# Optimization experiments

Hardware: AMD Instinct MI355X
Metric: run time of the kernel (lower is better)

Reference implementation:

```python
import jax, jax.numpy as jnp
import numpy as np

B, H, W = 4, 112, 112
N = H * W              # 12544 tokens
NBHD = 48              # local neighborhood size
DIM = 256
OUT_DIM = 512
INNER = 4              # inner_ch of weight_net
TABLE = 4096           # pre_table rows
ALPHA = 4.0
DS_RATE = 0.25
STRIDE = 2
RESERVE = (H // 4) * (W // 4)  # 784 reserve tokens (pos % 4 == 0)
EPS = 1e-5


def _ln(x, g, b):
    m = x.mean(-1, keepdims=True)
    v = ((x - m) ** 2).mean(-1, keepdims=True)
    return (x - m) / jnp.sqrt(v + EPS) * g + b


def setup_inputs() -> dict:
    key = jax.random.key(0)
    ks = jax.random.split(key, 8)
    ii, jj = jnp.meshgrid(jnp.arange(H), jnp.arange(W), indexing='ij')
    pos = jnp.stack([ii, jj], -1).reshape(1, N, 2).astype(jnp.float32)
    pos = jnp.tile(pos, (B, 1, 1))                             # b x n x 2 integer grid
    feat = jax.random.normal(ks[0], (B, N, DIM), jnp.float32)
    member_idx = jax.random.randint(ks[1], (B, N, NBHD), 0, N)
    cluster_mask = (jax.random.uniform(ks[2], (B, N, NBHD)) > 0.1).astype(jnp.float32)
    learned_prob = jax.random.uniform(ks[3], (B, N, 1), dtype=jnp.float32)
    pe_idx = jax.random.randint(ks[4], (B, N, NBHD), 0, TABLE)
    pre_table = jax.random.normal(ks[5], (TABLE, 5), jnp.float32)
    w1 = jax.random.normal(ks[6], (5, INNER), jnp.float32) * 0.4
    b1 = jnp.zeros((INNER,), jnp.float32)
    ln1_g = jnp.ones((INNER,), jnp.float32)
    ln1_b = jnp.zeros((INNER,), jnp.float32)
    norm_g = jnp.ones((INNER * DIM,), jnp.float32)
    norm_b = jnp.zeros((INNER * DIM,), jnp.float32)
    lin_w = jax.random.normal(ks[7], (INNER * DIM, OUT_DIM), jnp.float32) * (1.0 / np.sqrt(INNER * DIM))
    lin_b = jnp.zeros((OUT_DIM,), jnp.float32)
    return dict(pos=pos, feat=feat, member_idx=member_idx, cluster_mask=cluster_mask,
                learned_prob=learned_prob, stride=STRIDE, pe_idx=pe_idx, reserve_num=RESERVE,
                pre_table=pre_table, w1=w1, b1=b1, ln1_g=ln1_g, ln1_b=ln1_b,
                norm_g=norm_g, norm_b=norm_b, lin_w=lin_w, lin_b=lin_b)


def reference(pos, feat, member_idx, cluster_mask, learned_prob, stride, pe_idx,
              reserve_num, pre_table, w1, b1, ln1_g, ln1_b, norm_g, norm_b, lin_w, lin_b):
    b, n, c = feat.shape
    keep_num = int(n * DS_RATE)
    pos_long = pos.astype(jnp.int32)
    # stride == 2 branch: tokens on the coarse grid get prob 1
    grid_prob = jnp.all(pos_long % stride == 0, axis=-1).astype(jnp.float32)      # b x n
    lp_s = jax.lax.stop_gradient(learned_prob).reshape(b, n) * ALPHA              # detached scores
    final_prob = grid_prob + lp_s
    reserve_mask = jnp.all(pos_long % (stride * 2) == 0, axis=-1).astype(jnp.float32)
    final_prob = final_prob + reserve_mask * (-100.0)
    sample_num = keep_num - reserve_num
    _, sample_idx = jax.lax.top_k(final_prob, sample_num)                         # b x sample_num
    # per-row nonzero of reserve_mask (exactly reserve_num hits per row)
    flat_nz = jnp.nonzero(reserve_mask.reshape(-1) > 0, size=b * reserve_num)[0]
    reserve_idx = (flat_nz % n).reshape(b, reserve_num).astype(sample_idx.dtype)
    idx = jnp.concatenate([sample_idx, reserve_idx], axis=1)                      # b x keep_num

    pos_k = jnp.take_along_axis(pos, idx[:, :, None], axis=1)                     # b x keep x 2
    nbhd = member_idx.shape[-1]
    mem_k = jnp.take_along_axis(member_idx, idx[:, :, None], axis=1)              # b x keep x nbhd
    pe_k = jnp.take_along_axis(pe_idx, idx[:, :, None], axis=1)
    cm_k = jnp.take_along_axis(cluster_mask, idx[:, :, None], axis=1)
    lp = jnp.take_along_axis(learned_prob, mem_k.reshape(b, -1, 1), axis=1)
    lp = lp.reshape(b, keep_num, nbhd, 1)

    # weight_net on the small PE table, then gather per-edge weights
    wt = jax.nn.gelu(_ln(pre_table @ w1 + b1, ln1_g, ln1_b), approximate=False)   # TABLE x INNER
    weights = wt[pe_k]                                                            # b x keep x nbhd x INNER
    weights = weights * (lp * cm_k[..., None])

    # CLUSTENWF: gather neighbor features and weighted-sum over the neighborhood
    gathered = jnp.take_along_axis(feat, mem_k.reshape(b, -1, 1), axis=1)
    gathered = gathered.reshape(b, keep_num, nbhd, c)                             # b x keep x nbhd x c
    out = jnp.einsum('bnkm,bnkc->bnmc', weights, gathered).reshape(b, keep_num, INNER * c)
    out = _ln(out, norm_g, norm_b)
    return pos_k, out @ lin_w + lin_b
```

## Files before the change

### kernel.cpp

```cpp
#include <hip/hip_runtime.h>

typedef unsigned short u16;
typedef unsigned int u32;
typedef unsigned long long u64;

#define NB 4
#define NTOK 12544
#define NBHD 48
#define DIM 256
#define OUTD 512
#define KEEPN 3136
#define SAMPLEN 2352
#define RESN 784
#define GW 112
#define TABLE 4096
#define POSN (NB * KEEPN * 2)
#define QTR (NTOK / 4)
#define NBKT 16384

#define BLKM 128
#define BLKN 256
#define BROW 40

#define FEATB_BYTES (25690112ull)
#define XWS_BYTES   (25690112ull)
#define LINT_BYTES  (1048576ull)
#define KEYS_BYTES  (401408ull)
#define PART_BYTES  (802816ull)
#define WS_NEED (FEATB_BYTES + XWS_BYTES + LINT_BYTES + KEYS_BYTES + PART_BYTES)

__device__ __forceinline__ float bf2f(u16 u) {
    union { u32 i; float f; } v; v.i = ((u32)u) << 16; return v.f;
}
__device__ __forceinline__ float asf(u32 u) {
    union { u32 i; float f; } v; v.i = u; return v.f;
}
__device__ __forceinline__ u16 f2bf(float f) {
    union { u32 i; float f; } v; v.f = f;
    return (u16)((v.i + 0x7FFFu + ((v.i >> 16) & 1u)) >> 16);
}

typedef __bf16 bf16x8 __attribute__((ext_vector_type(8)));
typedef float floatx4 __attribute__((ext_vector_type(4)));
typedef float floatx2 __attribute__((ext_vector_type(2)));

__device__ __forceinline__ float make_f(float lp, int n) {
    int i = n / GW, j = n % GW;
    float f = lp * 4.0f;
    if (((i | j) & 1) == 0) f = 1.0f + f;
    if (((i | j) & 3) == 0) f = f + (-100.0f);
    return f;
}
__device__ __forceinline__ u64 f_to_key(float f, int n) {
    union { float f; u32 u; } v; v.f = f;
    u32 m = (v.u & 0x80000000u) ? ~v.u : (v.u | 0x80000000u);
    return (((u64)m) << 32) | (u64)(0xFFFFFFFFu - (u32)n);
}
__device__ __forceinline__ int f_to_bucket(float f) {
    int b = (int)floorf(f * 3276.8f);
    return b < 0 ? 0 : (b > NBKT - 1 ? NBKT - 1 : b);
}

__global__ __launch_bounds__(256) void prep_kernel(
    const float* __restrict__ feat, u16* __restrict__ featb,
    const float* __restrict__ lin_w, u16* __restrict__ linT,
    u32* __restrict__ hist,
    const float* __restrict__ pre_table, const float* __restrict__ w1,
    const float* __restrict__ b1, const float* __restrict__ g1,
    const float* __restrict__ bb1, float* __restrict__ wt) {
    __shared__ u16 T[64 * 65];
    int bid = blockIdx.x;
    int t = threadIdx.x;
    if (bid >= 128) {
        int ft = (bid - 128) * 256 + t;
        float4 v = ((const float4*)feat)[ft];
        u64 w = (u64)f2bf(v.x) | ((u64)f2bf(v.y) << 16) |
                ((u64)f2bf(v.z) << 32) | ((u64)f2bf(v.w) << 48);
        ((u64*)featb)[ft] = w;
        return;
    }
    int bx = bid & 15, by = bid >> 4;
    int k0 = bx * 64, n0 = by * 64;
    hist[bid * 512 + t] = 0;
    hist[bid * 512 + 256 + t] = 0;
    int gid = bid * 256 + t;
    if (gid < TABLE) {
        float z[4];
#pragma unroll
        for (int m = 0; m < 4; ++m) {
            float acc = b1[m];
#pragma unroll
            for (int d = 0; d < 5; ++d) acc += pre_table[gid * 5 + d] * w1[d * 4 + m];
            z[m] = acc;
        }
        float mean = (z[0] + z[1] + z[2] + z[3]) * 0.25f;
        float var = 0.0f;
#pragma unroll
        for (int m = 0; m < 4; ++m) { float d = z[m] - mean; var += d * d; }
        float rstd = rsqrtf(var * 0.25f + 1e-5f);
        float wv[4];
#pragma unroll
        for (int m = 0; m < 4; ++m) {
            float y = (z[m] - mean) * rstd * g1[m] + bb1[m];
            wv[m] = 0.5f * y * (1.0f + erff(y * 0.70710678118654752f));
        }
        *(float4*)&wt[gid * 4] = make_float4(wv[0], wv[1], wv[2], wv[3]);
    }
    int r = t >> 2, c4 = (t & 3) * 16;
#pragma unroll
    for (int i = 0; i < 4; ++i) {
        float4 v = *(const float4*)&lin_w[(size_t)(k0 + r) * OUTD + n0 + c4 + i * 4];
        T[(c4 + i * 4 + 0) * 65 + r] = f2bf(v.x);
        T[(c4 + i * 4 + 1) * 65 + r] = f2bf(v.y);
        T[(c4 + i * 4 + 2) * 65 + r] = f2bf(v.z);
        T[(c4 + i * 4 + 3) * 65 + r] = f2bf(v.w);
    }
    __syncthreads();
    int nl = t >> 2, kc = (t & 3) * 16;
    union { uint4 v[2]; u16 h[16]; } u;
#pragma unroll
    for (int i = 0; i < 16; ++i) u.h[i] = T[nl * 65 + kc + i];
    u16* dst = &linT[(size_t)(n0 + nl) * 1024 + k0 + kc];
    *(uint4*)(dst + 0) = u.v[0];
    *(uint4*)(dst + 8) = u.v[1];
}

__global__ __launch_bounds__(256) void hist_kernel(
    const float* __restrict__ lprob, u32* __restrict__ hist) {
    int g = blockIdx.x * 256 + threadIdx.x;
    int b = g / NTOK, n = g % NTOK;
    int bkt = f_to_bucket(make_f(lprob[g], n));
    atomicAdd(&hist[b * NBKT + bkt], 1u);
}

__global__ __launch_bounds__(1024) void prefix_kernel(
    const u32* __restrict__ hist, u32* __restrict__ base, u32* __restrict__ cursor) {
    int b = blockIdx.x, t = threadIdx.x;
    const u32* h = hist + b * NBKT;
    u32 loc[16], own = 0;
#pragma unroll
    for (int i = 0; i < 16; ++i) { loc[i] = h[t * 16 + i]; own += loc[i]; }
    __shared__ u32 buf[2][1024];
    buf[0][t] = own;
    __syncthreads();
    int src = 0;
    for (int off = 1; off < 1024; off <<= 1) {
        u32 v = buf[src][t] + ((t + off < 1024) ? buf[src][t + off] : 0u);
        buf[src ^ 1][t] = v;
        src ^= 1;
        __syncthreads();
    }
    u32 above = buf[src][t] - own;
    u32 suf = 0, bout[16];
    for (int i = 15; i >= 0; --i) { bout[i] = above + suf; suf += loc[i]; }
    u32* bb = base + b * NBKT;
    u32* cc = cursor + b * NBKT;
#pragma unroll
    for (int i = 0; i < 16; ++i) { bb[t * 16 + i] = bout[i]; cc[t * 16 + i] = bout[i]; }
}

__global__ __launch_bounds__(256) void scatter_kernel(
    const float* __restrict__ lprob, u32* __restrict__ cursor,
    u64* __restrict__ slots) {
    int g = blockIdx.x * 256 + threadIdx.x;
    int b = g / NTOK, n = g % NTOK;
    float f = make_f(lprob[g], n);
    int bkt = f_to_bucket(f);
    u32 s = atomicAdd(&cursor[b * NBKT + bkt], 1u);
    slots[b * NTOK + s] = f_to_key(f, n);
}

__global__ __launch_bounds__(256) void rank_finalize_kernel(
    const float* __restrict__ lprob, const u32* __restrict__ hist,
    const u32* __restrict__ base, const u64* __restrict__ slots,
    float* __restrict__ pos_out) {
    int g = blockIdx.x * 256 + threadIdx.x;
    int b = g / NTOK, n = g % NTOK;
    int i = n / GW, j = n % GW;
    if (((i | j) & 3) == 0) {
        int r = (i >> 2) * 28 + (j >> 2);
        int slot = b * KEEPN + SAMPLEN + r;
        pos_out[slot * 2 + 0] = (float)i;
        pos_out[slot * 2 + 1] = (float)j;
        return;
    }
    float f = make_f(lprob[g], n);
    int bkt = f_to_bucket(f);
    u32 r0 = base[b * NBKT + bkt];
    if (r0 >= SAMPLEN) return;
    u64 my = f_to_key(f, n);
    u32 cnt = hist[b * NBKT + bkt];
    const u64* sl = slots + b * NTOK + r0;
    u32 rank = r0;
    for (u32 s = 0; s < cnt; ++s) rank += (sl[s] > my) ? 1u : 0u;
    if (rank < SAMPLEN) {
        int slot = b * KEEPN + (int)rank;
        pos_out[slot * 2 + 0] = (float)i;
        pos_out[slot * 2 + 1] = (float)j;
    }
}

__global__ __launch_bounds__(1024, 2) void token_v10_kernel(
    const float* __restrict__ pos_in, u16* __restrict__ xdst,
    const int* __restrict__ member_idx, const int* __restrict__ pe_idx,
    const float* __restrict__ cmask, const float* __restrict__ lprob,
    const u16* __restrict__ featb, const float* __restrict__ wt,
    const float* __restrict__ norm_g, const float* __restrict__ norm_b) {
    int bi = blockIdx.x;
    int xcd = bi & 7, jj = bi >> 3;
    int b = xcd >> 1;
    int tid = threadIdx.x;
    int wave = tid >> 6, lane = tid & 63;
    int t = b * KEEPN + (xcd & 1) * 1568 + jj * 16 + wave;

    __shared__ float4 w_s[16][NBHD];

    float2 pp = *(const float2*)&pos_in[t * 2];
    int n_src = (int)pp.x * GW + (int)pp.y;

    u32 moffb = 0;
    if (lane < NBHD) {
        int e = (b * NTOK + n_src) * NBHD + lane;
        int mem = member_idx[e];
        float sc = lprob[b * NTOK + mem] * cmask[e];
        float4 w4 = *(const float4*)&wt[pe_idx[e] * 4];
        w_s[wave][lane] = make_float4(w4.x * sc, w4.y * sc, w4.z * sc, w4.w * sc);
        moffb = (u32)mem * (DIM * 2);
    }
    __syncthreads();

    floatx2 accA[4] = {};
    floatx2 accB[4] = {};
    const char* fb = (const char*)featb + (size_t)b * NTOK * DIM * 2;
    u32 lane8 = (u32)lane * 8;
#pragma unroll
    for (int k = 0; k < NBHD; ++k) {
        u32 mk = (u32)__builtin_amdgcn_readlane((int)moffb, k);
        uint2 d = *(const uint2*)(fb + mk + lane8);
        float4 w = w_s[wave][k];
        floatx2 w01 = {w.x, w.y};
        floatx2 w23 = {w.z, w.w};
        float c0 = asf(d.x << 16);
        float c1 = asf(d.x & 0xFFFF0000u);
        float c2 = asf(d.y << 16);
        float c3 = asf(d.y & 0xFFFF0000u);
        floatx2 c0v = {c0, c0}, c1v = {c1, c1}, c2v = {c2, c2}, c3v = {c3, c3};
        accA[0] = __builtin_elementwise_fma(w01, c0v, accA[0]);
        accB[0] = __builtin_elementwise_fma(w23, c0v, accB[0]);
        accA[1] = __builtin_elementwise_fma(w01, c1v, accA[1]);
        accB[1] = __builtin_elementwise_fma(w23, c1v, accB[1]);
        accA[2] = __builtin_elementwise_fma(w01, c2v, accA[2]);
        accB[2] = __builtin_elementwise_fma(w23, c2v, accB[2]);
        accA[3] = __builtin_elementwise_fma(w01, c3v, accA[3]);
        accB[3] = __builtin_elementwise_fma(w23, c3v, accB[3]);
    }

    float s1 = 0.0f, s2 = 0.0f;
#pragma unroll
    for (int j = 0; j < 4; ++j) {
        float v0 = accA[j][0], v1 = accA[j][1], v2 = accB[j][0], v3 = accB[j][1];
        s1 += v0 + v1 + v2 + v3;
        s2 += v0 * v0 + v1 * v1 + v2 * v2 + v3 * v3;
    }
#pragma unroll
    for (int off = 32; off > 0; off >>= 1) {
        s1 += __shfl_xor(s1, off, 64);
        s2 += __shfl_xor(s2, off, 64);
    }
    float mean = s1 * (1.0f / 1024.0f);
    float var = fmaxf(s2 * (1.0f / 1024.0f) - mean * mean, 0.0f);
    float rstd = rsqrtf(var + 1e-5f);

    u16* Xp = xdst + (size_t)t * 1024;
#pragma unroll
    for (int m = 0; m < 4; ++m) {
        int cc = m * 256 + lane * 4;
        float4 g4 = *(const float4*)&norm_g[cc];
        float4 b4 = *(const float4*)&norm_b[cc];
        float v0 = (m == 0) ? accA[0][0] : (m == 1) ? accA[0][1]
                 : (m == 2) ? accB[0][0] : accB[0][1];
        float v1 = (m == 0) ? accA[1][0] : (m == 1) ? accA[1][1]
                 : (m == 2) ? accB[1][0] : accB[1][1];
        float v2 = (m == 0) ? accA[2][0] : (m == 1) ? accA[2][1]
                 : (m == 2) ? accB[2][0] : accB[2][1];
        float v3 = (m == 0) ? accA[3][0] : (m == 1) ? accA[3][1]
                 : (m == 2) ? accB[3][0] : accB[3][1];
        u16 h0 = f2bf((v0 - mean) * rstd * g4.x + b4.x);
        u16 h1 = f2bf((v1 - mean) * rstd * g4.y + b4.y);
        u16 h2 = f2bf((v2 - mean) * rstd * g4.z + b4.z);
        u16 h3 = f2bf((v3 - mean) * rstd * g4.w + b4.w);
        u64 w = (u64)h0 | ((u64)h1 << 16) | ((u64)h2 << 32) | ((u64)h3 << 48);
        *(u64*)(Xp + cc) = w;
    }
}

#define GROW 40
__global__ __launch_bounds__(256) void gemm_tile_kernel(
    const u16* __restrict__ xws, const u16* __restrict__ linT,
    const float* __restrict__ lin_b, float* __restrict__ out) {
    __shared__ __align__(16) u16 As[128 * GROW];
    __shared__ __align__(16) u16 Bs[64 * GROW];
    int bid = blockIdx.x;
    int xcd = bid & 7, c = bid >> 3;
    int tile = xcd * 98 + c;
    int m0 = (tile >> 3) * 128, n0 = (tile & 7) * 64;

    int tid = threadIdx.x;
    int wave = tid >> 6, lane = tid & 63;
    int l15 = lane & 15, quad = lane >> 4;
    int wm = wave >> 1, wn = wave & 1;
    int sr = tid >> 2, sk = (tid & 3) * 8;

    const u16* Ap0 = xws + (size_t)(m0 + sr) * 1024 + sk;
    const u16* Ap1 = Ap0 + (size_t)64 * 1024;
    const u16* Bp0 = linT + (size_t)(n0 + sr) * 1024 + sk;

    uint4 a0 = *(const uint4*)(Ap0);
    uint4 a1 = *(const uint4*)(Ap1);
    uint4 b0 = *(const uint4*)(Bp0);

    floatx4 acc[4][2] = {};
    for (int kk = 0; kk < 1024; kk += 32) {
        __syncthreads();
        *(uint4*)&As[sr * GROW + sk] = a0;
        *(uint4*)&As[(64 + sr) * GROW + sk] = a1;
        *(uint4*)&Bs[sr * GROW + sk] = b0;
        __syncthreads();
        if (kk + 32 < 1024) {
            a0 = *(const uint4*)(Ap0 + kk + 32);
            a1 = *(const uint4*)(Ap1 + kk + 32);
            b0 = *(const uint4*)(Bp0 + kk + 32);
        }
        bf16x8 af[4], bfv[2];
#pragma unroll
        for (int mi = 0; mi < 4; ++mi)
            af[mi] = *(const bf16x8*)&As[(wm * 64 + mi * 16 + l15) * GROW + quad * 8];
#pragma unroll
        for (int ni = 0; ni < 2; ++ni)
            bfv[ni] = *(const bf16x8*)&Bs[(wn * 32 + ni * 16 + l15) * GROW + quad * 8];
#pragma unroll
        for (int mi = 0; mi < 4; ++mi)
#pragma unroll
            for (int ni = 0; ni < 2; ++ni)
                acc[mi][ni] = __builtin_amdgcn_mfma_f32_16x16x32_bf16(
                    af[mi], bfv[ni], acc[mi][ni], 0, 0, 0);
    }
#pragma unroll
    for (int ni = 0; ni < 2; ++ni) {
        int col = n0 + wn * 32 + ni * 16 + l15;
        float bias = lin_b[col];
#pragma unroll
        for (int mi = 0; mi < 4; ++mi)
#pragma unroll
            for (int reg = 0; reg < 4; ++reg) {
                int row = m0 + wm * 64 + mi * 16 + quad * 4 + reg;
                out[(size_t)row * OUTD + col] = acc[mi][ni][reg] + bias;
            }
    }
}

__global__ __launch_bounds__(256) void key_kernel(
    const float* __restrict__ lprob, u64* __restrict__ keys) {
    int g = blockIdx.x * 256 + threadIdx.x;
    int n = g % NTOK;
    keys[g] = f_to_key(make_f(lprob[g], n), n);
}

__global__ __launch_bounds__(256) void partial_rank_kernel(
    const u64* __restrict__ keys, u32* __restrict__ part) {
    int b = blockIdx.y, z = blockIdx.z;
    int n = blockIdx.x * 256 + threadIdx.x;
    u64 my = keys[b * NTOK + n];
    const u64* kb = keys + b * NTOK + z * QTR;
    u32 cnt = 0;
    for (int t = 0; t < QTR; t += 8) {
#pragma unroll
        for (int j = 0; j < 8; ++j) cnt += (kb[t + j] > my) ? 1u : 0u;
    }
    part[(z * NB + b) * NTOK + n] = cnt;
}

__global__ __launch_bounds__(256) void finalize_kernel(
    const u32* __restrict__ part, float* __restrict__ pos_out) {
    int b = blockIdx.y;
    int n = blockIdx.x * 256 + threadIdx.x;
    int g = b * NTOK + n;
    u32 rank = part[g] + part[(NB + b) * NTOK + n] +
               part[(2 * NB + b) * NTOK + n] + part[(3 * NB + b) * NTOK + n];
    int i = n / GW, j = n % GW;
    if (rank < SAMPLEN) {
        int slot = b * KEEPN + (int)rank;
        pos_out[slot * 2 + 0] = (float)i;
        pos_out[slot * 2 + 1] = (float)j;
    }
    if (((i | j) & 3) == 0) {
        int r = (i >> 2) * 28 + (j >> 2);
        int slot = b * KEEPN + SAMPLEN + r;
        pos_out[slot * 2 + 0] = (float)i;
        pos_out[slot * 2 + 1] = (float)j;
    }
}

__global__ __launch_bounds__(256) void token_fb_kernel(
    const float* __restrict__ pos_in, u16* __restrict__ xdst,
    const int* __restrict__ member_idx, const int* __restrict__ pe_idx,
    const float* __restrict__ cmask, const float* __restrict__ lprob,
    const float* __restrict__ featf, const float* __restrict__ pre_table,
    const float* __restrict__ w1, const float* __restrict__ b1,
    const float* __restrict__ g1, const float* __restrict__ bb1,
    const float* __restrict__ norm_g, const float* __restrict__ norm_b) {
    int t = blockIdx.x;
    int b = t / KEEPN;
    int tid = threadIdx.x;
    __shared__ int mem_s[NBHD];
    __shared__ float4 w_s[NBHD];
    __shared__ float red[10];

    int n_src = (int)pos_in[t * 2 + 0] * GW + (int)pos_in[t * 2 + 1];

    if (tid < NBHD) {
        int e = (b * NTOK + n_src) * NBHD + tid;
        int mem = member_idx[e];
        int pe = pe_idx[e];
        float cm = cmask[e];
        float lpe = lprob[b * NTOK + mem];
        float z[4];
#pragma unroll
        for (int m = 0; m < 4; ++m) {
            float acc = b1[m];
#pragma unroll
            for (int d = 0; d < 5; ++d) acc += pre_table[pe * 5 + d] * w1[d * 4 + m];
            z[m] = acc;
        }
        float mean = (z[0] + z[1] + z[2] + z[3]) * 0.25f;
        float var = 0.0f;
#pragma unroll
        for (int m = 0; m < 4; ++m) { float d = z[m] - mean; var += d * d; }
        float rstd = rsqrtf(var * 0.25f + 1e-5f);
        float sc = lpe * cm;
        float wv[4];
#pragma unroll
        for (int m = 0; m < 4; ++m) {
            float y = (z[m] - mean) * rstd * g1[m] + bb1[m];
            wv[m] = 0.5f * y * (1.0f + erff(y * 0.70710678118654752f)) * sc;
        }
        w_s[tid] = make_float4(wv[0], wv[1], wv[2], wv[3]);
        mem_s[tid] = mem;
    }
    __syncthreads();

    float a0 = 0.f, a1 = 0.f, a2 = 0.f, a3 = 0.f;
    size_t base = (size_t)b * NTOK * DIM + tid;
#pragma unroll 8
    for (int k = 0; k < NBHD; ++k) {
        float g = featf[base + (size_t)mem_s[k] * DIM];
        float4 w = w_s[k];
        a0 += w.x * g; a1 += w.y * g; a2 += w.z * g; a3 += w.w * g;
    }
    float s1 = a0 + a1 + a2 + a3;
    float s2 = a0 * a0 + a1 * a1 + a2 * a2 + a3 * a3;
#pragma unroll
    for (int off = 32; off > 0; off >>= 1) {
        s1 += __shfl_down(s1, off, 64);
        s2 += __shfl_down(s2, off, 64);
    }
    int wave = tid >> 6, lane = tid & 63;
    if (lane == 0) { red[wave] = s1; red[4 + wave] = s2; }
    __syncthreads();
    if (tid == 0) {
        float S = red[0] + red[1] + red[2] + red[3];
        float Q = red[4] + red[5] + red[6] + red[7];
        float mean = S * (1.0f / 1024.0f);
        float var = fmaxf(Q * (1.0f / 1024.0f) - mean * mean, 0.0f);
        red[8] = mean; red[9] = rsqrtf(var + 1e-5f);
    }
    __syncthreads();
    float mean = red[8], rstd = red[9];
    float acc4[4] = {a0, a1, a2, a3};
    u16* Xp = xdst + (size_t)t * 1024;
#pragma unroll
    for (int m = 0; m < 4; ++m) {
        int cc = m * 256 + tid;
        float v = (acc4[m] - mean) * rstd * norm_g[cc] + norm_b[cc];
        Xp[cc] = f2bf(v);
    }
}

__global__ __launch_bounds__(256) void gemm_inplace_kernel(
    const float* __restrict__ lin_w, const float* __restrict__ lin_b,
    float* __restrict__ out) {
    __shared__ __align__(16) u16 Bs[BLKN * BROW];
    int tile_m = blockIdx.x;
    int nblk = blockIdx.y;
    int tid = threadIdx.x;
    int wave = tid >> 6, lane = tid & 63;
    int l15 = lane & 15, quad = lane >> 4;

    const u16* Xbase = (const u16*)out;
    floatx4 acc[8][4] = {};

    for (int kk = 0; kk < 1024; kk += 32) {
        __syncthreads();
#pragma unroll
        for (int it = 0; it < 4; ++it) {
            int task = it * 256 + tid;
            int kp = task >> 6;
            int ng = task & 63;
            int k = kp * 2;
            int n0 = nblk * BLKN + ng * 4;
            float4 fa = *(const float4*)&lin_w[(size_t)(kk + k) * OUTD + n0];
            float4 fb = *(const float4*)&lin_w[(size_t)(kk + k + 1) * OUTD + n0];
            u16* bp = &Bs[(ng * 4) * BROW + k];
            *(u32*)(bp + 0 * BROW) = (u32)f2bf(fa.x) | ((u32)f2bf(fb.x) << 16);
            *(u32*)(bp + 1 * BROW) = (u32)f2bf(fa.y) | ((u32)f2bf(fb.y) << 16);
            *(u32*)(bp + 2 * BROW) = (u32)f2bf(fa.z) | ((u32)f2bf(fb.z) << 16);
            *(u32*)(bp + 3 * BROW) = (u32)f2bf(fa.w) | ((u32)f2bf(fb.w) << 16);
        }
        __syncthreads();
        bf16x8 bfrag[4];
#pragma unroll
        for (int ni = 0; ni < 4; ++ni)
            bfrag[ni] = *(const bf16x8*)&Bs[(wave * 64 + ni * 16 + l15) * BROW + quad * 8];
#pragma unroll
        for (int mi = 0; mi < 8; ++mi) {
            int row = tile_m * BLKM + mi * 16 + l15;
            bf16x8 af = *(const bf16x8*)&Xbase[(size_t)row * 1024 + kk + quad * 8];
#pragma unroll
            for (int ni = 0; ni < 4; ++ni)
                acc[mi][ni] = __builtin_amdgcn_mfma_f32_16x16x32_bf16(
                    af, bfrag[ni], acc[mi][ni], 0, 0, 0);
        }
    }
    __syncthreads();
#pragma unroll
    for (int mi = 0; mi < 8; ++mi)
#pragma unroll
        for (int ni = 0; ni < 4; ++ni) {
            int col = nblk * BLKN + wave * 64 + ni * 16 + l15;
            float bias = lin_b[col];
#pragma unroll
            for (int reg = 0; reg < 4; ++reg) {
                int row = tile_m * BLKM + mi * 16 + quad * 4 + reg;
                out[(size_t)row * OUTD + col] = acc[mi][ni][reg] + bias;
            }
        }
}

extern "C" void kernel_launch(void* const* d_in, const int* in_sizes, int n_in,
                              void* d_out, int out_size, void* d_ws, size_t ws_size,
                              hipStream_t stream) {
    const float* feat     = (const float*)d_in[1];
    const int* member_idx = (const int*)d_in[2];
    const float* cmask    = (const float*)d_in[3];
    const float* lprob    = (const float*)d_in[4];
    const int* pe_idx     = (const int*)d_in[6];
    const float* pre_table= (const float*)d_in[8];
    const float* w1       = (const float*)d_in[9];
    const float* b1       = (const float*)d_in[10];
    const float* g1       = (const float*)d_in[11];
    const float* bb1      = (const float*)d_in[12];
    const float* norm_g   = (const float*)d_in[13];
    const float* norm_b   = (const float*)d_in[14];
    const float* lin_w    = (const float*)d_in[15];
    const float* lin_b    = (const float*)d_in[16];

    float* pos_out = (float*)d_out;
    float* out     = pos_out + POSN;

    if (ws_size >= WS_NEED) {
        char* ws = (char*)d_ws;
        u16* featb = (u16*)ws;
        u16* xws   = (u16*)(ws + FEATB_BYTES);
        u16* linT  = (u16*)(ws + FEATB_BYTES + XWS_BYTES);
        u64* slots = (u64*)(ws + FEATB_BYTES + XWS_BYTES + LINT_BYTES);
        u32* hist  = (u32*)(ws + FEATB_BYTES + XWS_BYTES + LINT_BYTES + KEYS_BYTES);
        u32* base  = hist + NB * NBKT;
        u32* curs  = base + NB * NBKT;
        float* wtbuf = out;

        prep_kernel<<<12672, 256, 0, stream>>>(
            feat, featb, lin_w, linT, hist, pre_table, w1, b1, g1, bb1, wtbuf);
        hist_kernel<<<(NB * NTOK) / 256, 256, 0, stream>>>(lprob, hist);
        prefix_kernel<<<NB, 1024, 0, stream>>>(hist, base, curs);
        scatter_kernel<<<(NB * NTOK) / 256, 256, 0, stream>>>(lprob, curs, slots);
        rank_finalize_kernel<<<(NB * NTOK) / 256, 256, 0, stream>>>(
            lprob, hist, base, slots, pos_out);
        token_v10_kernel<<<784, 1024, 0, stream>>>(
            pos_out, xws, member_idx, pe_idx, cmask, lprob, featb,
            wtbuf, norm_g, norm_b);
        gemm_tile_kernel<<<784, 256, 0, stream>>>(xws, linT, lin_b, out);
    } else {
        u64* keys = (u64*)out;
        u32* part = (u32*)((char*)out + 401408);

        key_kernel<<<(NB * NTOK) / 256, 256, 0, stream>>>(lprob, keys);
        partial_rank_kernel<<<dim3(49, NB, 4), 256, 0, stream>>>(keys, part);
        finalize_kernel<<<dim3(49, NB), 256, 0, stream>>>(part, pos_out);
        token_fb_kernel<<<NB * KEEPN, 256, 0, stream>>>(
            pos_out, (u16*)out, member_idx, pe_idx, cmask, lprob, feat,
            pre_table, w1, b1, g1, bb1, norm_g, norm_b);
        gemm_inplace_kernel<<<dim3(98, 2), 256, 0, stream>>>(lin_w, lin_b, out);
    }
}
```

Baseline: 245.3 us.

## Stage neighbor feature rows into LDS via async global_load_lds in two phases

The token aggregation kernel now copies the 48 gathered bf16 neighbor rows into LDS with direct global-to-LDS loads, issued as two batches of 24 rows. The second batch is issued after the first batch's compute, replacing per-iteration dependent global loads in the FMA loop. Blocks shrink from 1024 to 256 threads (4 tokens per block) to fit a roughly 48KB staging buffer per block. The aim is more memory-level parallelism for the irregular gather. The risk is lower occupancy from the LDS footprint, and overlap is limited because the second batch is waited on immediately.

New measurement: 248.3 us. No clear change (+1.2%).

```diff
diff --git a/kernel.cpp b/kernel.cpp
--- a/kernel.cpp
+++ b/kernel.cpp
@@ -43,6 +43,13 @@
 typedef __bf16 bf16x8 __attribute__((ext_vector_type(8)));
 typedef float floatx4 __attribute__((ext_vector_type(4)));
 typedef float floatx2 __attribute__((ext_vector_type(2)));
+
+__device__ __forceinline__ void gld_lds16(const void* g, void* l) {
+    __builtin_amdgcn_global_load_lds(
+        (const __attribute__((address_space(1))) void*)g,
+        (__attribute__((address_space(3))) void*)l,
+        16, 0, 0);
+}
 
 __device__ __forceinline__ float make_f(float lp, int n) {
     int i = n / GW, j = n % GW;
@@ -200,7 +207,7 @@
     }
 }
 
-__global__ __launch_bounds__(1024, 2) void token_v10_kernel(
+__global__ __launch_bounds__(256) void token_v11_kernel(
     const float* __restrict__ pos_in, u16* __restrict__ xdst,
     const int* __restrict__ member_idx, const int* __restrict__ pe_idx,
     const float* __restrict__ cmask, const float* __restrict__ lprob,
@@ -211,9 +218,10 @@
     int b = xcd >> 1;
     int tid = threadIdx.x;
     int wave = tid >> 6, lane = tid & 63;
-    int t = b * KEEPN + (xcd & 1) * 1568 + jj * 16 + wave;
-
-    __shared__ float4 w_s[16][NBHD];
+    int t = b * KEEPN + (xcd & 1) * 1568 + jj * 4 + wave;
+
+    __shared__ float4 w_s[4][NBHD];
+    __shared__ __align__(16) u16 stage[4][24 * 256];
 
     float2 pp = *(const float2*)&pos_in[t * 2];
     int n_src = (int)pp.x * GW + (int)pp.y;
@@ -227,32 +235,60 @@
         w_s[wave][lane] = make_float4(w4.x * sc, w4.y * sc, w4.z * sc, w4.w * sc);
         moffb = (u32)mem * (DIM * 2);
     }
+
+    const char* fb = (const char*)featb + (size_t)b * NTOK * DIM * 2;
+    u32 lsub = (u32)(lane & 31) * 16;
+    int hi = lane >> 5;
+
+#pragma unroll
+    for (int p = 0; p < 12; ++p) {
+        u32 m1 = (u32)__builtin_amdgcn_readlane((int)moffb, 2 * p);
+        u32 m2 = (u32)__builtin_amdgcn_readlane((int)moffb, 2 * p + 1);
+        u32 mo = hi ? m2 : m1;
+        gld_lds16(fb + mo + lsub, &stage[wave][p * 512]);
+    }
     __syncthreads();
 
     floatx2 accA[4] = {};
     floatx2 accB[4] = {};
-    const char* fb = (const char*)featb + (size_t)b * NTOK * DIM * 2;
-    u32 lane8 = (u32)lane * 8;
-#pragma unroll
-    for (int k = 0; k < NBHD; ++k) {
-        u32 mk = (u32)__builtin_amdgcn_readlane((int)moffb, k);
-        uint2 d = *(const uint2*)(fb + mk + lane8);
-        float4 w = w_s[wave][k];
-        floatx2 w01 = {w.x, w.y};
-        floatx2 w23 = {w.z, w.w};
-        float c0 = asf(d.x << 16);
-        float c1 = asf(d.x & 0xFFFF0000u);
-        float c2 = asf(d.y << 16);
-        float c3 = asf(d.y & 0xFFFF0000u);
-        floatx2 c0v = {c0, c0}, c1v = {c1, c1}, c2v = {c2, c2}, c3v = {c3, c3};
-        accA[0] = __builtin_elementwise_fma(w01, c0v, accA[0]);
-        accB[0] = __builtin_elementwise_fma(w23, c0v, accB[0]);
-        accA[1] = __builtin_elementwise_fma(w01, c1v, accA[1]);
-        accB[1] = __builtin_elementwise_fma(w23, c1v, accB[1]);
-        accA[2] = __builtin_elementwise_fma(w01, c2v, accA[2]);
-        accB[2] = __builtin_elementwise_fma(w23, c2v, accB[2]);
-        accA[3] = __builtin_elementwise_fma(w01, c3v, accA[3]);
-        accB[3] = __builtin_elementwise_fma(w23, c3v, accB[3]);
+    int lane4 = lane * 4;
+
+#pragma unroll
+    for (int ph = 0; ph < 2; ++ph) {
+        int ck = ph * 24;
+        asm volatile("s_waitcnt vmcnt(0)" ::: "memory");
+        __builtin_amdgcn_sched_barrier(0);
+#pragma unroll
+        for (int k = 0; k < 24; ++k) {
+            uint2 d = *(const uint2*)&stage[wave][k * 256 + lane4];
+            float4 w = w_s[wave][ck + k];
+            floatx2 w01 = {w.x, w.y};
+            floatx2 w23 = {w.z, w.w};
+            float c0 = asf(d.x << 16);
+            float c1 = asf(d.x & 0xFFFF0000u);
+            float c2 = asf(d.y << 16);
+            float c3 = asf(d.y & 0xFFFF0000u);
+            floatx2 c0v = {c0, c0}, c1v = {c1, c1}, c2v = {c2, c2}, c3v = {c3, c3};
+            accA[0] = __builtin_elementwise_fma(w01, c0v, accA[0]);
+            accB[0] = __builtin_elementwise_fma(w23, c0v, accB[0]);
+            accA[1] = __builtin_elementwise_fma(w01, c1v, accA[1]);
+            accB[1] = __builtin_elementwise_fma(w23, c1v, accB[1]);
+            accA[2] = __builtin_elementwise_fma(w01, c2v, accA[2]);
+            accB[2] = __builtin_elementwise_fma(w23, c2v, accB[2]);
+            accA[3] = __builtin_elementwise_fma(w01, c3v, accA[3]);
+            accB[3] = __builtin_elementwise_fma(w23, c3v, accB[3]);
+        }
+        if (ph == 0) {
+            asm volatile("s_waitcnt lgkmcnt(0)" ::: "memory");
+            __builtin_amdgcn_sched_barrier(0);
+#pragma unroll
+            for (int p = 0; p < 12; ++p) {
+                u32 m1 = (u32)__builtin_amdgcn_readlane((int)moffb, 24 + 2 * p);
+                u32 m2 = (u32)__builtin_amdgcn_readlane((int)moffb, 24 + 2 * p + 1);
+                u32 mo = hi ? m2 : m1;
+                gld_lds16(fb + mo + lsub, &stage[wave][p * 512]);
+            }
+        }
     }
 
     float s1 = 0.0f, s2 = 0.0f;
@@ -585,7 +621,7 @@
         scatter_kernel<<<(NB * NTOK) / 256, 256, 0, stream>>>(lprob, curs, slots);
         rank_finalize_kernel<<<(NB * NTOK) / 256, 256, 0, stream>>>(
             lprob, hist, base, slots, pos_out);
-        token_v10_kernel<<<784, 1024, 0, stream>>>(
+        token_v11_kernel<<<(NB * KEEPN) / 4, 256, 0, stream>>>(
             pos_out, xws, member_idx, pe_idx, cmask, lprob, featb,
             wtbuf, norm_g, norm_b);
         gemm_tile_kernel<<<784, 256, 0, stream>>>(xws, linT, lin_b, out);
```
